# Kernel optimization log

Measured on AMD Instinct MI355X. Metric: run time of the kernel, lower is better.

The kernel has to match this reference:

```python
import jax, jax.numpy as jnp
import numpy as np

B, N, H = 8, 256, 64
L = 2          # n_layers
A = 10         # n_actions
EPS = 1e-5


def _layernorm(x, g, b):
    m = jnp.mean(x, axis=-1, keepdims=True)
    v = jnp.mean(jnp.square(x - m), axis=-1, keepdims=True)
    return (x - m) * jax.lax.rsqrt(v + EPS) * g + b


def setup_inputs() -> dict:
    key = jax.random.key(0)
    ks = jax.random.split(key, 12)
    s = 0.05
    return {
        "X": jax.random.normal(ks[0], (B, N, H), dtype=jnp.float32),
        "E": jax.random.normal(ks[1], (B, N, N, H), dtype=jnp.float32),
        # per-layer weights, stacked over layers (torch Linear: y = x @ W.T)
        "W3": jax.random.normal(ks[2], (L, H, H), dtype=jnp.float32) * s,
        "W4": jax.random.normal(ks[3], (L, H, H), dtype=jnp.float32) * s,
        "W5": jax.random.normal(ks[4], (L, H, H), dtype=jnp.float32) * s,
        "W6": jax.random.normal(ks[5], (L, H, H), dtype=jnp.float32) * s,
        "ln_ng": jnp.ones((L, H), dtype=jnp.float32),
        "ln_nb": jnp.zeros((L, H), dtype=jnp.float32),
        "ln_eg": jnp.ones((L, H), dtype=jnp.float32),
        "ln_eb": jnp.zeros((L, H), dtype=jnp.float32),
        "hw1": jax.random.normal(ks[6], (H, H), dtype=jnp.float32) * s,
        "hb1": jnp.zeros((H,), dtype=jnp.float32),
        "hw2": jax.random.normal(ks[7], (A, H), dtype=jnp.float32) * s,
        "hb2": jnp.zeros((A,), dtype=jnp.float32),
    }


def reference(X, E, W3, W4, W5, W6, ln_ng, ln_nb, ln_eg, ln_eb, hw1, hb1, hw2, hb2):
    # in_proj / edge_proj are Identity (in_dim == edge_dim == hid_dim)
    for l in range(L):
        Xi = X @ W3[l].T                       # (B,n,H)
        E_hat = E @ W4[l].T                    # (B,n,n,H)
        # (Xi_exp + Xj_exp + E_hat).sum(-1) == Xi.sum(-1)[:,:,None] + Xi.sum(-1)[:,None,:] + E_hat.sum(-1)
        s = jnp.sum(Xi, axis=-1)               # (B,n)
        att_logits = s[:, :, None] + s[:, None, :] + jnp.sum(E_hat, axis=-1)
        att = jax.nn.softmax(att_logits, axis=-1)[..., None]  # (B,n,n,1)
        E_next = E_hat * att                   # (B,n,n,H)
        Xj = X @ W5[l].T                       # (B,n,H)
        agg = jnp.einsum('bijh,bjh->bih', E_next, Xj)
        X_res = X @ W6[l].T
        X = _layernorm(jax.nn.relu(agg + X_res), ln_ng[l], ln_nb[l]) + X
        E = _layernorm(E_next, ln_eg[l], ln_eb[l])
        # dropout p=0.0 -> identity
    h = jax.nn.relu(X @ hw1.T + hb1)
    return h @ hw2.T + hb2                     # (B,n,n_actions)
```

## Files before the change

kernel.cpp:

```cpp
#include <hip/hip_runtime.h>
#include <hip/hip_bf16.h>

#define NB 256
#define HH 64

using short8 = __attribute__((ext_vector_type(8))) short;
using f4     = __attribute__((ext_vector_type(4))) float;

static __device__ __forceinline__ unsigned short f2bfbits(float f) {
    __hip_bfloat16 h = __float2bfloat16(f);
    return __builtin_bit_cast(unsigned short, h);
}

static __device__ __forceinline__ void split8(const float* v, short8& hi, short8& lo) {
    unsigned int hd[4], ld[4];
    #pragma unroll
    for (int j = 0; j < 4; ++j) {
        unsigned int u0 = __builtin_bit_cast(unsigned int, v[2*j]);
        unsigned int u1 = __builtin_bit_cast(unsigned int, v[2*j+1]);
        hd[j] = (u1 & 0xFFFF0000u) | (u0 >> 16);
        float r0 = v[2*j]   - __builtin_bit_cast(float, u0 & 0xFFFF0000u);
        float r1 = v[2*j+1] - __builtin_bit_cast(float, u1 & 0xFFFF0000u);
        ld[j] = ((unsigned int)f2bfbits(r1) << 16) | (unsigned int)f2bfbits(r0);
    }
    uint4 h4; h4.x = hd[0]; h4.y = hd[1]; h4.z = hd[2]; h4.w = hd[3];
    uint4 l4; l4.x = ld[0]; l4.y = ld[1]; l4.z = ld[2]; l4.w = ld[3];
    hi = __builtin_bit_cast(short8, h4);
    lo = __builtin_bit_cast(short8, l4);
}

static __device__ __forceinline__ short8 ld_frag_pair(const char* base, int idx0) {
    uint2 a = *reinterpret_cast<const uint2*>(base + (size_t)idx0 * 8);
    uint2 b = *reinterpret_cast<const uint2*>(base + (size_t)idx0 * 8 + 128);
    uint4 u; u.x = a.x; u.y = a.y; u.z = b.x; u.w = b.y;
    return __builtin_bit_cast(short8, u);
}

__global__ __launch_bounds__(256)
void setup_kernel(const float* __restrict__ W3, const float* __restrict__ W4,
                  float* __restrict__ w3s, uint4* __restrict__ w4tab) {
    const int t = threadIdx.x;
    if (blockIdx.x == 0) {
        if (t < 128) {
            const int l = t >> 6, k = t & 63;
            float s = 0.f;
            for (int h = 0; h < 64; ++h) s += W3[(size_t)(l*64 + h)*64 + k];
            w3s[t] = s;
        }
    } else {
        const int l = blockIdx.x - 1;
        const float* W4l = W4 + (size_t)l * 4096;
        uint4* tab = w4tab + (size_t)l * 1024;
        const int mt = t >> 6, lane = t & 63, m = lane & 15, q = lane >> 4;
        const float* row = W4l + (size_t)(mt*16 + m) * 64;
        #pragma unroll
        for (int ks = 0; ks < 2; ++ks) {
            float v[8];
            *reinterpret_cast<float4*>(&v[0]) = *reinterpret_cast<const float4*>(row + ks*32 + q*8);
            *reinterpret_cast<float4*>(&v[4]) = *reinterpret_cast<const float4*>(row + ks*32 + q*8 + 4);
            short8 hi, lo;
            split8(v, hi, lo);
            tab[(mt*4 + ks)*64 + lane]     = __builtin_bit_cast(uint4, hi);
            tab[(mt*4 + 2 + ks)*64 + lane] = __builtin_bit_cast(uint4, lo);
        }
    }
}

__global__ __launch_bounds__(256)
void prep_kernel(const float* __restrict__ Xsrc,
                 const float* __restrict__ w3s,
                 const float* __restrict__ W5l,
                 const float* __restrict__ W6l,
                 float* __restrict__ s_ws,
                 float* __restrict__ Xjf,
                 float* __restrict__ Xres_ws)
{
    __shared__ float w5s[64*65];
    __shared__ float w6s[64*65];
    const int t = threadIdx.x;
    #pragma unroll
    for (int j = 0; j < 4; ++j) {
        const int fidx = j*1024 + t*4;
        float4 v5 = *reinterpret_cast<const float4*>(W5l + fidx);
        float4 v6 = *reinterpret_cast<const float4*>(W6l + fidx);
        const int row = fidx >> 6, col = fidx & 63;
        w5s[row*65+col+0] = v5.x; w5s[row*65+col+1] = v5.y;
        w5s[row*65+col+2] = v5.z; w5s[row*65+col+3] = v5.w;
        w6s[row*65+col+0] = v6.x; w6s[row*65+col+1] = v6.y;
        w6s[row*65+col+2] = v6.z; w6s[row*65+col+3] = v6.w;
    }
    __syncthreads();

    const int w = t >> 6, lane = t & 63;
    const int r = blockIdx.x * 4 + w;
    float xr[64];
    #pragma unroll
    for (int k = 0; k < 16; ++k) {
        float4 v = *reinterpret_cast<const float4*>(Xsrc + (size_t)r*64 + k*4);
        xr[k*4+0] = v.x; xr[k*4+1] = v.y; xr[k*4+2] = v.z; xr[k*4+3] = v.w;
    }
    float aj = 0.f, ar = 0.f;
    #pragma unroll
    for (int k = 0; k < 64; ++k) {
        aj += xr[k] * w5s[lane*65 + k];
        ar += xr[k] * w6s[lane*65 + k];
    }
    const int b = r >> 8, j = r & 255;
    const int wj = j >> 6, jt = (j >> 4) & 3, m = j & 15;
    const int mt = lane >> 4, q = (lane >> 2) & 3, ri = lane & 3;
    Xjf[(size_t)b*16384 + (size_t)(((wj*4 + jt)*4 + mt)*64 + (q*16 + m))*4 + ri] = aj;
    Xres_ws[(size_t)r*64 + lane] = ar;
    float sv = xr[lane] * w3s[lane];
    #pragma unroll
    for (int d = 1; d < 64; d <<= 1) sv += __shfl_xor(sv, d, 64);
    if (lane == 0) s_ws[r] = sv;
}

template<bool FIRST>
__global__ __launch_bounds__(256)
void layer_kernel(void* Ebuf,
                  const float* __restrict__ s_ws,
                  const float* __restrict__ Xjf,
                  const float* __restrict__ Xres_ws,
                  const float* __restrict__ Xold,
                  float* __restrict__ Xnext,
                  const uint4* __restrict__ w4tab,
                  const float* __restrict__ eg,
                  const float* __restrict__ eb,
                  const float* __restrict__ ng,
                  const float* __restrict__ nb)
{
    __shared__ float att[NB];
    __shared__ float red[8];
    __shared__ float agg_lds[4][64];

    const int bi  = blockIdx.x;
    const int b   = bi >> 8;
    const int tid = threadIdx.x;
    const int w   = tid >> 6;
    const int lane = tid & 63;
    const int m = lane & 15;
    const int q = lane >> 4;

    char* ebase = (char*)Ebuf + (size_t)bi * 65536;

    short8 aH[4][2], aL[4][2];
    #pragma unroll
    for (int mt = 0; mt < 4; ++mt) {
        aH[mt][0] = __builtin_bit_cast(short8, w4tab[(mt*4 + 0)*64 + lane]);
        aH[mt][1] = __builtin_bit_cast(short8, w4tab[(mt*4 + 1)*64 + lane]);
        aL[mt][0] = __builtin_bit_cast(short8, w4tab[(mt*4 + 2)*64 + lane]);
        aL[mt][1] = __builtin_bit_cast(short8, w4tab[(mt*4 + 3)*64 + lane]);
    }

    f4 acc[4][4] = {};

    #pragma unroll
    for (int jt = 0; jt < 4; ++jt) {
        short8 bh0, bl0, bh1, bl1;
        if constexpr (FIRST) {
            const float* er = (const float*)ebase + (size_t)(w*64 + jt*16 + m) * 64;
            float v0[8], v1[8];
            *reinterpret_cast<float4*>(&v0[0]) = *reinterpret_cast<const float4*>(er + q*8);
            *reinterpret_cast<float4*>(&v0[4]) = *reinterpret_cast<const float4*>(er + q*8 + 4);
            *reinterpret_cast<float4*>(&v1[0]) = *reinterpret_cast<const float4*>(er + 32 + q*8);
            *reinterpret_cast<float4*>(&v1[4]) = *reinterpret_cast<const float4*>(er + 32 + q*8 + 4);
            split8(v0, bh0, bl0);
            split8(v1, bh1, bl1);
        } else {
            const char* hiP = ebase;
            const char* loP = ebase + 32768;
            const int col = (q & 1)*32 + m;
            const int base0 = ((w*4 + jt)*4)*64;
            const int mt0 = (q >> 1);
            bh0 = ld_frag_pair(hiP, base0 + mt0*64 + col);
            bh1 = ld_frag_pair(hiP, base0 + (2 + mt0)*64 + col);
            bl0 = ld_frag_pair(loP, base0 + mt0*64 + col);
            bl1 = ld_frag_pair(loP, base0 + (2 + mt0)*64 + col);
        }
        #pragma unroll
        for (int mt = 0; mt < 4; ++mt) {
            acc[mt][jt] = __builtin_amdgcn_mfma_f32_16x16x32_bf16(aH[mt][0], bh0, acc[mt][jt], 0, 0, 0);
            acc[mt][jt] = __builtin_amdgcn_mfma_f32_16x16x32_bf16(aL[mt][0], bh0, acc[mt][jt], 0, 0, 0);
            acc[mt][jt] = __builtin_amdgcn_mfma_f32_16x16x32_bf16(aH[mt][0], bl0, acc[mt][jt], 0, 0, 0);
            acc[mt][jt] = __builtin_amdgcn_mfma_f32_16x16x32_bf16(aH[mt][1], bh1, acc[mt][jt], 0, 0, 0);
            acc[mt][jt] = __builtin_amdgcn_mfma_f32_16x16x32_bf16(aL[mt][1], bh1, acc[mt][jt], 0, 0, 0);
            acc[mt][jt] = __builtin_amdgcn_mfma_f32_16x16x32_bf16(aH[mt][1], bl1, acc[mt][jt], 0, 0, 0);
        }
    }

    #pragma unroll
    for (int jt = 0; jt < 4; ++jt) {
        float t = 0.f;
        #pragma unroll
        for (int mt = 0; mt < 4; ++mt)
            #pragma unroll
            for (int r = 0; r < 4; ++r) t += acc[mt][jt][r];
        t += __shfl_xor(t, 16, 64);
        t += __shfl_xor(t, 32, 64);
        if (lane < 16) att[w*64 + jt*16 + lane] = t;
    }
    __syncthreads();

    const float lj = att[tid] + s_ws[bi] + s_ws[b*NB + tid];
    float mx = lj;
    #pragma unroll
    for (int d = 1; d < 64; d <<= 1) mx = fmaxf(mx, __shfl_xor(mx, d, 64));
    if (lane == 0) red[w] = mx;
    __syncthreads();
    mx = fmaxf(fmaxf(red[0], red[1]), fmaxf(red[2], red[3]));
    const float ev = __expf(lj - mx);
    float sm = ev;
    #pragma unroll
    for (int d = 1; d < 64; d <<= 1) sm += __shfl_xor(sm, d, 64);
    if (lane == 0) red[4 + w] = sm;
    __syncthreads();
    sm = (red[4] + red[5]) + (red[6] + red[7]);
    att[tid] = ev / sm;
    __syncthreads();

    float attv[4];
    #pragma unroll
    for (int jt = 0; jt < 4; ++jt) attv[jt] = att[w*64 + jt*16 + m];
    #pragma unroll
    for (int mt = 0; mt < 4; ++mt)
        #pragma unroll
        for (int jt = 0; jt < 4; ++jt)
            #pragma unroll
            for (int r = 0; r < 4; ++r) acc[mt][jt][r] *= attv[jt];

    float mean[4], rstd[4];
    #pragma unroll
    for (int jt = 0; jt < 4; ++jt) {
        float s = 0.f, ss = 0.f;
        #pragma unroll
        for (int mt = 0; mt < 4; ++mt)
            #pragma unroll
            for (int r = 0; r < 4; ++r) { float v = acc[mt][jt][r]; s += v; ss += v*v; }
        s  += __shfl_xor(s, 16, 64);  s  += __shfl_xor(s, 32, 64);
        ss += __shfl_xor(ss, 16, 64); ss += __shfl_xor(ss, 32, 64);
        float mu = s * (1.f/64.f);
        mean[jt] = mu;
        rstd[jt] = rsqrtf(ss * (1.f/64.f) - mu*mu + 1e-5f);
    }

    float p[4][4] = {};
    #pragma unroll
    for (int jt = 0; jt < 4; ++jt) {
        #pragma unroll
        for (int mt = 0; mt < 4; ++mt) {
            float4 xv = *reinterpret_cast<const float4*>(
                Xjf + (size_t)b*16384 + (size_t)(((w*4 + jt)*4 + mt)*64 + lane)*4);
            p[mt][0] += acc[mt][jt][0] * xv.x;
            p[mt][1] += acc[mt][jt][1] * xv.y;
            p[mt][2] += acc[mt][jt][2] * xv.z;
            p[mt][3] += acc[mt][jt][3] * xv.w;
        }
    }
    #pragma unroll
    for (int d = 1; d < 16; d <<= 1)
        #pragma unroll
        for (int mt = 0; mt < 4; ++mt)
            #pragma unroll
            for (int r = 0; r < 4; ++r) p[mt][r] += __shfl_xor(p[mt][r], d, 64);
    if (m == 0) {
        #pragma unroll
        for (int mt = 0; mt < 4; ++mt) {
            float4 st = make_float4(p[mt][0], p[mt][1], p[mt][2], p[mt][3]);
            *reinterpret_cast<float4*>(&agg_lds[w][mt*16 + q*4]) = st;
        }
    }

    if constexpr (FIRST) {
        float egv[4][4], ebv[4][4];
        #pragma unroll
        for (int mt = 0; mt < 4; ++mt)
            #pragma unroll
            for (int r = 0; r < 4; ++r) {
                const int h = mt*16 + q*4 + r;
                egv[mt][r] = eg[h];
                ebv[mt][r] = eb[h];
            }
        char* hiP = ebase;
        char* loP = ebase + 32768;
        #pragma unroll
        for (int jt = 0; jt < 4; ++jt) {
            #pragma unroll
            for (int mt = 0; mt < 4; ++mt) {
                float o[4];
                #pragma unroll
                for (int r = 0; r < 4; ++r)
                    o[r] = (acc[mt][jt][r] - mean[jt]) * rstd[jt] * egv[mt][r] + ebv[mt][r];
                unsigned int u0 = __builtin_bit_cast(unsigned int, o[0]);
                unsigned int u1 = __builtin_bit_cast(unsigned int, o[1]);
                unsigned int u2 = __builtin_bit_cast(unsigned int, o[2]);
                unsigned int u3 = __builtin_bit_cast(unsigned int, o[3]);
                uint2 h2;
                h2.x = (u1 & 0xFFFF0000u) | (u0 >> 16);
                h2.y = (u3 & 0xFFFF0000u) | (u2 >> 16);
                float r0 = o[0] - __builtin_bit_cast(float, u0 & 0xFFFF0000u);
                float r1 = o[1] - __builtin_bit_cast(float, u1 & 0xFFFF0000u);
                float r2 = o[2] - __builtin_bit_cast(float, u2 & 0xFFFF0000u);
                float r3 = o[3] - __builtin_bit_cast(float, u3 & 0xFFFF0000u);
                uint2 l2;
                l2.x = ((unsigned int)f2bfbits(r1) << 16) | (unsigned int)f2bfbits(r0);
                l2.y = ((unsigned int)f2bfbits(r3) << 16) | (unsigned int)f2bfbits(r2);
                const int idxS = ((w*4 + jt)*4 + mt)*64 + lane;
                *reinterpret_cast<uint2*>(hiP + (size_t)idxS*8) = h2;
                *reinterpret_cast<uint2*>(loP + (size_t)idxS*8) = l2;
            }
        }
    }
    __syncthreads();

    if (w == 0) {
        float a = agg_lds[0][lane] + agg_lds[1][lane] + agg_lds[2][lane] + agg_lds[3][lane];
        float v = fmaxf(a + Xres_ws[(size_t)bi*64 + lane], 0.f);
        float s = v, ss = v*v;
        #pragma unroll
        for (int d = 1; d < 64; d <<= 1) { s += __shfl_xor(s, d, 64); ss += __shfl_xor(ss, d, 64); }
        float mu  = s * (1.f/64.f);
        float var = ss * (1.f/64.f) - mu*mu;
        Xnext[(size_t)bi*64 + lane] =
            (v - mu) * rsqrtf(var + 1e-5f) * ng[lane] + nb[lane] + Xold[(size_t)bi*64 + lane];
    }
}

__global__ __launch_bounds__(256)
void head_kernel(const float* __restrict__ Xf,
                 const float* __restrict__ hw1,
                 const float* __restrict__ hb1,
                 const float* __restrict__ hw2,
                 const float* __restrict__ hb2,
                 float* __restrict__ out)
{
    __shared__ float w1s[64*65];
    __shared__ float w2s[10*65];
    __shared__ float h1s[4][64];
    const int t = threadIdx.x;
    #pragma unroll
    for (int j = 0; j < 4; ++j) {
        const int fidx = j*1024 + t*4;
        float4 v = *reinterpret_cast<const float4*>(hw1 + fidx);
        const int row = fidx >> 6, col = fidx & 63;
        w1s[row*65+col+0] = v.x; w1s[row*65+col+1] = v.y;
        w1s[row*65+col+2] = v.z; w1s[row*65+col+3] = v.w;
    }
    if (t < 160) {
        const int fidx = t*4;
        float4 v = *reinterpret_cast<const float4*>(hw2 + fidx);
        const int row = fidx >> 6, col = fidx & 63;
        w2s[row*65+col+0] = v.x; w2s[row*65+col+1] = v.y;
        w2s[row*65+col+2] = v.z; w2s[row*65+col+3] = v.w;
    }
    __syncthreads();

    const int w = t >> 6, lane = t & 63;
    const int r = blockIdx.x * 4 + w;
    float xr[64];
    #pragma unroll
    for (int k = 0; k < 16; ++k) {
        float4 v = *reinterpret_cast<const float4*>(Xf + (size_t)r*64 + k*4);
        xr[k*4+0] = v.x; xr[k*4+1] = v.y; xr[k*4+2] = v.z; xr[k*4+3] = v.w;
    }
    float a = hb1[lane];
    #pragma unroll
    for (int k = 0; k < 64; ++k) a += xr[k] * w1s[lane*65 + k];
    h1s[w][lane] = fmaxf(a, 0.f);
    __syncthreads();
    if (lane < 10) {
        float o = hb2[lane];
        #pragma unroll
        for (int h = 0; h < 64; ++h) o += h1s[w][h] * w2s[lane*65 + h];
        out[(size_t)r*10 + lane] = o;
    }
}

extern "C" void kernel_launch(void* const* d_in, const int* in_sizes, int n_in,
                              void* d_out, int out_size, void* d_ws, size_t ws_size,
                              hipStream_t stream) {
    const float* X   = (const float*)d_in[0];
    void*        E   = (void*)d_in[1];
    const float* W3  = (const float*)d_in[2];
    const float* W4  = (const float*)d_in[3];
    const float* W5  = (const float*)d_in[4];
    const float* W6  = (const float*)d_in[5];
    const float* ng  = (const float*)d_in[6];
    const float* nbp = (const float*)d_in[7];
    const float* eg  = (const float*)d_in[8];
    const float* ebp = (const float*)d_in[9];
    const float* hw1 = (const float*)d_in[10];
    const float* hb1 = (const float*)d_in[11];
    const float* hw2 = (const float*)d_in[12];
    const float* hb2 = (const float*)d_in[13];
    float* outp = (float*)d_out;

    float* wsf   = (float*)d_ws;
    float* s_ws  = wsf;
    float* Xjf   = wsf + 2048;
    float* Xres  = wsf + 133120;
    float* Xa    = wsf + 264192;
    float* Xb    = wsf + 395264;
    float* w3s   = wsf + 526336;
    uint4* w4tab = (uint4*)(wsf + 526464);

    setup_kernel<<<3, 256, 0, stream>>>(W3, W4, w3s, w4tab);

    prep_kernel<<<512, 256, 0, stream>>>(X, w3s, W5, W6, s_ws, Xjf, Xres);
    layer_kernel<true><<<2048, 256, 0, stream>>>(E, s_ws, Xjf, Xres,
        X, Xa, w4tab, eg, ebp, ng, nbp);

    prep_kernel<<<512, 256, 0, stream>>>(Xa, w3s + 64, W5 + 4096, W6 + 4096,
        s_ws, Xjf, Xres);
    layer_kernel<false><<<2048, 256, 0, stream>>>(E, s_ws, Xjf, Xres,
        Xa, Xb, w4tab + 1024, eg + 64, ebp + 64, ng + 64, nbp + 64);

    head_kernel<<<512, 256, 0, stream>>>(Xb, hw1, hb1, hw2, hb2, outp);
}
```

Baseline: 309.4 us.

## Store layer-1 edges as single bf16, precompute layer-2 logits, fuse head and setup

Layer 1 now writes its normalized edge tensor back as a single bf16 copy instead of hi/lo split pairs, laid out so layer 2 can load fragments with one 16-byte load each. Layer 1 also computes the layer-2 attention logit row-sum directly, using column sums of W4[1]. Layer 2 therefore skips the logit reduction, the lo-part MFMAs and the edge LayerNorm, since its E output is never used. The setup kernel is folded into the first prep launch and the head MLP into the last layer kernel. Together this cuts E traffic, MFMA count and launch count, at the cost of reduced precision for layer-2 edges, which are rounded once to bf16.

```diff
diff --git a/kernel.cpp b/kernel.cpp
--- a/kernel.cpp
+++ b/kernel.cpp
@@ -11,16 +11,20 @@
     __hip_bfloat16 h = __float2bfloat16(f);
     return __builtin_bit_cast(unsigned short, h);
 }
+static __device__ __forceinline__ float bfbits2f(unsigned short u) {
+    unsigned int x = (unsigned int)u << 16;
+    return __builtin_bit_cast(float, x);
+}
 
 static __device__ __forceinline__ void split8(const float* v, short8& hi, short8& lo) {
     unsigned int hd[4], ld[4];
     #pragma unroll
     for (int j = 0; j < 4; ++j) {
-        unsigned int u0 = __builtin_bit_cast(unsigned int, v[2*j]);
-        unsigned int u1 = __builtin_bit_cast(unsigned int, v[2*j+1]);
-        hd[j] = (u1 & 0xFFFF0000u) | (u0 >> 16);
-        float r0 = v[2*j]   - __builtin_bit_cast(float, u0 & 0xFFFF0000u);
-        float r1 = v[2*j+1] - __builtin_bit_cast(float, u1 & 0xFFFF0000u);
+        unsigned short h0 = f2bfbits(v[2*j]);
+        unsigned short h1 = f2bfbits(v[2*j+1]);
+        hd[j] = ((unsigned int)h1 << 16) | (unsigned int)h0;
+        float r0 = v[2*j]   - bfbits2f(h0);
+        float r1 = v[2*j+1] - bfbits2f(h1);
         ld[j] = ((unsigned int)f2bfbits(r1) << 16) | (unsigned int)f2bfbits(r0);
     }
     uint4 h4; h4.x = hd[0]; h4.y = hd[1]; h4.z = hd[2]; h4.w = hd[3];
@@ -29,29 +33,31 @@
     lo = __builtin_bit_cast(short8, l4);
 }
 
-static __device__ __forceinline__ short8 ld_frag_pair(const char* base, int idx0) {
-    uint2 a = *reinterpret_cast<const uint2*>(base + (size_t)idx0 * 8);
-    uint2 b = *reinterpret_cast<const uint2*>(base + (size_t)idx0 * 8 + 128);
-    uint4 u; u.x = a.x; u.y = a.y; u.z = b.x; u.w = b.y;
-    return __builtin_bit_cast(short8, u);
-}
-
+template<bool BUILD>
 __global__ __launch_bounds__(256)
-void setup_kernel(const float* __restrict__ W3, const float* __restrict__ W4,
-                  float* __restrict__ w3s, uint4* __restrict__ w4tab) {
+void prep_kernel(const float* __restrict__ Xsrc,
+                 const float* __restrict__ W3l,
+                 const float* __restrict__ W5l,
+                 const float* __restrict__ W6l,
+                 const float* __restrict__ W4all,
+                 uint4* __restrict__ w4tab,
+                 float* __restrict__ w41cs,
+                 float* __restrict__ s_ws,
+                 float* __restrict__ Xjf,
+                 float* __restrict__ Xres_ws)
+{
+    __shared__ float w5s[64*65];
+    __shared__ float w6s[64*65];
+    __shared__ float csl[4][64];
+    __shared__ float cst[64];
     const int t = threadIdx.x;
-    if (blockIdx.x == 0) {
-        if (t < 128) {
-            const int l = t >> 6, k = t & 63;
-            float s = 0.f;
-            for (int h = 0; h < 64; ++h) s += W3[(size_t)(l*64 + h)*64 + k];
-            w3s[t] = s;
-        }
-    } else {
-        const int l = blockIdx.x - 1;
-        const float* W4l = W4 + (size_t)l * 4096;
+    const int w = t >> 6, lane = t & 63;
+
+    if (BUILD && blockIdx.x >= 512) {
+        const int l = blockIdx.x - 512;
+        const float* W4l = W4all + (size_t)l * 4096;
         uint4* tab = w4tab + (size_t)l * 1024;
-        const int mt = t >> 6, lane = t & 63, m = lane & 15, q = lane >> 4;
+        const int mt = w, m = lane & 15, q = lane >> 4;
         const float* row = W4l + (size_t)(mt*16 + m) * 64;
         #pragma unroll
         for (int ks = 0; ks < 2; ++ks) {
@@ -63,24 +69,20 @@
             tab[(mt*4 + ks)*64 + lane]     = __builtin_bit_cast(uint4, hi);
             tab[(mt*4 + 2 + ks)*64 + lane] = __builtin_bit_cast(uint4, lo);
         }
-    }
-}
-
-__global__ __launch_bounds__(256)
-void prep_kernel(const float* __restrict__ Xsrc,
-                 const float* __restrict__ w3s,
-                 const float* __restrict__ W5l,
-                 const float* __restrict__ W6l,
-                 float* __restrict__ s_ws,
-                 float* __restrict__ Xjf,
-                 float* __restrict__ Xres_ws)
-{
-    __shared__ float w5s[64*65];
-    __shared__ float w6s[64*65];
-    const int t = threadIdx.x;
-    #pragma unroll
-    for (int j = 0; j < 4; ++j) {
-        const int fidx = j*1024 + t*4;
+        if (l == 1) {
+            float p = 0.f;
+            #pragma unroll
+            for (int i = 0; i < 16; ++i) p += W4l[(size_t)(w*16 + i)*64 + lane];
+            csl[w][lane] = p;
+            __syncthreads();
+            if (t < 64) w41cs[t] = (csl[0][t] + csl[1][t]) + (csl[2][t] + csl[3][t]);
+        }
+        return;
+    }
+
+    #pragma unroll
+    for (int jj = 0; jj < 4; ++jj) {
+        const int fidx = jj*1024 + t*4;
         float4 v5 = *reinterpret_cast<const float4*>(W5l + fidx);
         float4 v6 = *reinterpret_cast<const float4*>(W6l + fidx);
         const int row = fidx >> 6, col = fidx & 63;
@@ -89,9 +91,14 @@
         w6s[row*65+col+0] = v6.x; w6s[row*65+col+1] = v6.y;
         w6s[row*65+col+2] = v6.z; w6s[row*65+col+3] = v6.w;
     }
-    __syncthreads();
-
-    const int w = t >> 6, lane = t & 63;
+    float pcs = 0.f;
+    #pragma unroll
+    for (int i = 0; i < 16; ++i) pcs += W3l[(size_t)(w*16 + i)*64 + lane];
+    csl[w][lane] = pcs;
+    __syncthreads();
+    if (t < 64) cst[t] = (csl[0][t] + csl[1][t]) + (csl[2][t] + csl[3][t]);
+    __syncthreads();
+
     const int r = blockIdx.x * 4 + w;
     float xr[64];
     #pragma unroll
@@ -110,13 +117,13 @@
     const int mt = lane >> 4, q = (lane >> 2) & 3, ri = lane & 3;
     Xjf[(size_t)b*16384 + (size_t)(((wj*4 + jt)*4 + mt)*64 + (q*16 + m))*4 + ri] = aj;
     Xres_ws[(size_t)r*64 + lane] = ar;
-    float sv = xr[lane] * w3s[lane];
+    float sv = xr[lane] * cst[lane];
     #pragma unroll
     for (int d = 1; d < 64; d <<= 1) sv += __shfl_xor(sv, d, 64);
     if (lane == 0) s_ws[r] = sv;
 }
 
-template<bool FIRST>
+template<bool FIRST, bool LAST>
 __global__ __launch_bounds__(256)
 void layer_kernel(void* Ebuf,
                   const float* __restrict__ s_ws,
@@ -125,14 +132,22 @@
                   const float* __restrict__ Xold,
                   float* __restrict__ Xnext,
                   const uint4* __restrict__ w4tab,
+                  const float* __restrict__ w41cs,
                   const float* __restrict__ eg,
                   const float* __restrict__ eb,
                   const float* __restrict__ ng,
-                  const float* __restrict__ nb)
+                  const float* __restrict__ nb,
+                  const float* __restrict__ hw1,
+                  const float* __restrict__ hb1,
+                  const float* __restrict__ hw2,
+                  const float* __restrict__ hb2,
+                  float* __restrict__ outp)
 {
     __shared__ float att[NB];
     __shared__ float red[8];
     __shared__ float agg_lds[4][64];
+    __shared__ float w1s[LAST ? 64*65 : 1];
+    __shared__ float w2s[LAST ? 10*65 : 1];
 
     const int bi  = blockIdx.x;
     const int b   = bi >> 8;
@@ -144,65 +159,109 @@
 
     char* ebase = (char*)Ebuf + (size_t)bi * 65536;
 
-    short8 aH[4][2], aL[4][2];
+    float4 rawf[FIRST ? 4 : 1][FIRST ? 4 : 1];
+    uint4  rawb[FIRST ? 1 : 4][FIRST ? 1 : 2];
+    if constexpr (FIRST) {
+        #pragma unroll
+        for (int jt = 0; jt < 4; ++jt) {
+            const float* er = (const float*)ebase + (size_t)(w*64 + jt*16 + m) * 64;
+            rawf[jt][0] = *reinterpret_cast<const float4*>(er + q*8);
+            rawf[jt][1] = *reinterpret_cast<const float4*>(er + q*8 + 4);
+            rawf[jt][2] = *reinterpret_cast<const float4*>(er + 32 + q*8);
+            rawf[jt][3] = *reinterpret_cast<const float4*>(er + 32 + q*8 + 4);
+        }
+    } else {
+        #pragma unroll
+        for (int jt = 0; jt < 4; ++jt)
+            #pragma unroll
+            for (int ks = 0; ks < 2; ++ks)
+                rawb[jt][ks] = *reinterpret_cast<const uint4*>(
+                    ebase + (size_t)(((w*4 + jt)*2 + ks)*64 + lane) * 16);
+    }
+
+    if constexpr (LAST) {
+        #pragma unroll
+        for (int jj = 0; jj < 4; ++jj) {
+            const int fidx = jj*1024 + tid*4;
+            float4 v = *reinterpret_cast<const float4*>(hw1 + fidx);
+            const int row = fidx >> 6, col = fidx & 63;
+            w1s[row*65+col+0] = v.x; w1s[row*65+col+1] = v.y;
+            w1s[row*65+col+2] = v.z; w1s[row*65+col+3] = v.w;
+        }
+        if (tid < 160) {
+            const int fidx = tid*4;
+            float4 v = *reinterpret_cast<const float4*>(hw2 + fidx);
+            const int row = fidx >> 6, col = fidx & 63;
+            w2s[row*65+col+0] = v.x; w2s[row*65+col+1] = v.y;
+            w2s[row*65+col+2] = v.z; w2s[row*65+col+3] = v.w;
+        }
+    }
+
+    short8 aH[4][2];
+    short8 aL[FIRST ? 4 : 1][FIRST ? 2 : 1];
     #pragma unroll
     for (int mt = 0; mt < 4; ++mt) {
         aH[mt][0] = __builtin_bit_cast(short8, w4tab[(mt*4 + 0)*64 + lane]);
         aH[mt][1] = __builtin_bit_cast(short8, w4tab[(mt*4 + 1)*64 + lane]);
-        aL[mt][0] = __builtin_bit_cast(short8, w4tab[(mt*4 + 2)*64 + lane]);
-        aL[mt][1] = __builtin_bit_cast(short8, w4tab[(mt*4 + 3)*64 + lane]);
+        if constexpr (FIRST) {
+            aL[mt][0] = __builtin_bit_cast(short8, w4tab[(mt*4 + 2)*64 + lane]);
+            aL[mt][1] = __builtin_bit_cast(short8, w4tab[(mt*4 + 3)*64 + lane]);
+        }
     }
 
     f4 acc[4][4] = {};
 
     #pragma unroll
     for (int jt = 0; jt < 4; ++jt) {
-        short8 bh0, bl0, bh1, bl1;
         if constexpr (FIRST) {
-            const float* er = (const float*)ebase + (size_t)(w*64 + jt*16 + m) * 64;
+            short8 bh0, bl0, bh1, bl1;
             float v0[8], v1[8];
-            *reinterpret_cast<float4*>(&v0[0]) = *reinterpret_cast<const float4*>(er + q*8);
-            *reinterpret_cast<float4*>(&v0[4]) = *reinterpret_cast<const float4*>(er + q*8 + 4);
-            *reinterpret_cast<float4*>(&v1[0]) = *reinterpret_cast<const float4*>(er + 32 + q*8);
-            *reinterpret_cast<float4*>(&v1[4]) = *reinterpret_cast<const float4*>(er + 32 + q*8 + 4);
+            *reinterpret_cast<float4*>(&v0[0]) = rawf[jt][0];
+            *reinterpret_cast<float4*>(&v0[4]) = rawf[jt][1];
+            *reinterpret_cast<float4*>(&v1[0]) = rawf[jt][2];
+            *reinterpret_cast<float4*>(&v1[4]) = rawf[jt][3];
             split8(v0, bh0, bl0);
             split8(v1, bh1, bl1);
+            #pragma unroll
+            for (int mt = 0; mt < 4; ++mt) {
+                acc[mt][jt] = __builtin_amdgcn_mfma_f32_16x16x32_bf16(aH[mt][0], bh0, acc[mt][jt], 0, 0, 0);
+                acc[mt][jt] = __builtin_amdgcn_mfma_f32_16x16x32_bf16(aL[mt][0], bh0, acc[mt][jt], 0, 0, 0);
+                acc[mt][jt] = __builtin_amdgcn_mfma_f32_16x16x32_bf16(aH[mt][0], bl0, acc[mt][jt], 0, 0, 0);
+                acc[mt][jt] = __builtin_amdgcn_mfma_f32_16x16x32_bf16(aH[mt][1], bh1, acc[mt][jt], 0, 0, 0);
+                acc[mt][jt] = __builtin_amdgcn_mfma_f32_16x16x32_bf16(aL[mt][1], bh1, acc[mt][jt], 0, 0, 0);
+                acc[mt][jt] = __builtin_amdgcn_mfma_f32_16x16x32_bf16(aH[mt][1], bl1, acc[mt][jt], 0, 0, 0);
+            }
         } else {
-            const char* hiP = ebase;
-            const char* loP = ebase + 32768;
-            const int col = (q & 1)*32 + m;
-            const int base0 = ((w*4 + jt)*4)*64;
-            const int mt0 = (q >> 1);
-            bh0 = ld_frag_pair(hiP, base0 + mt0*64 + col);
-            bh1 = ld_frag_pair(hiP, base0 + (2 + mt0)*64 + col);
-            bl0 = ld_frag_pair(loP, base0 + mt0*64 + col);
-            bl1 = ld_frag_pair(loP, base0 + (2 + mt0)*64 + col);
-        }
-        #pragma unroll
-        for (int mt = 0; mt < 4; ++mt) {
-            acc[mt][jt] = __builtin_amdgcn_mfma_f32_16x16x32_bf16(aH[mt][0], bh0, acc[mt][jt], 0, 0, 0);
-            acc[mt][jt] = __builtin_amdgcn_mfma_f32_16x16x32_bf16(aL[mt][0], bh0, acc[mt][jt], 0, 0, 0);
-            acc[mt][jt] = __builtin_amdgcn_mfma_f32_16x16x32_bf16(aH[mt][0], bl0, acc[mt][jt], 0, 0, 0);
-            acc[mt][jt] = __builtin_amdgcn_mfma_f32_16x16x32_bf16(aH[mt][1], bh1, acc[mt][jt], 0, 0, 0);
-            acc[mt][jt] = __builtin_amdgcn_mfma_f32_16x16x32_bf16(aL[mt][1], bh1, acc[mt][jt], 0, 0, 0);
-            acc[mt][jt] = __builtin_amdgcn_mfma_f32_16x16x32_bf16(aH[mt][1], bl1, acc[mt][jt], 0, 0, 0);
-        }
-    }
-
-    #pragma unroll
-    for (int jt = 0; jt < 4; ++jt) {
-        float t = 0.f;
-        #pragma unroll
-        for (int mt = 0; mt < 4; ++mt)
-            #pragma unroll
-            for (int r = 0; r < 4; ++r) t += acc[mt][jt][r];
-        t += __shfl_xor(t, 16, 64);
-        t += __shfl_xor(t, 32, 64);
-        if (lane < 16) att[w*64 + jt*16 + lane] = t;
-    }
-    __syncthreads();
-
-    const float lj = att[tid] + s_ws[bi] + s_ws[b*NB + tid];
+            short8 b0 = __builtin_bit_cast(short8, rawb[jt][0]);
+            short8 b1 = __builtin_bit_cast(short8, rawb[jt][1]);
+            #pragma unroll
+            for (int mt = 0; mt < 4; ++mt) {
+                acc[mt][jt] = __builtin_amdgcn_mfma_f32_16x16x32_bf16(aH[mt][0], b0, acc[mt][jt], 0, 0, 0);
+                acc[mt][jt] = __builtin_amdgcn_mfma_f32_16x16x32_bf16(aH[mt][1], b1, acc[mt][jt], 0, 0, 0);
+            }
+        }
+    }
+
+    float lj;
+    if constexpr (FIRST) {
+        #pragma unroll
+        for (int jt = 0; jt < 4; ++jt) {
+            float t = 0.f;
+            #pragma unroll
+            for (int mt = 0; mt < 4; ++mt)
+                #pragma unroll
+                for (int r = 0; r < 4; ++r) t += acc[mt][jt][r];
+            t += __shfl_xor(t, 16, 64);
+            t += __shfl_xor(t, 32, 64);
+            if (lane < 16) att[w*64 + jt*16 + lane] = t;
+        }
+        __syncthreads();
+        lj = att[tid] + s_ws[bi] + s_ws[b*NB + tid];
+    } else {
+        const float* t1g = (const float*)(ebase + 32768);
+        lj = t1g[tid] + s_ws[bi] + s_ws[b*NB + tid];
+    }
+
     float mx = lj;
     #pragma unroll
     for (int d = 1; d < 64; d <<= 1) mx = fmaxf(mx, __shfl_xor(mx, d, 64));
@@ -228,21 +287,6 @@
         for (int jt = 0; jt < 4; ++jt)
             #pragma unroll
             for (int r = 0; r < 4; ++r) acc[mt][jt][r] *= attv[jt];
-
-    float mean[4], rstd[4];
-    #pragma unroll
-    for (int jt = 0; jt < 4; ++jt) {
-        float s = 0.f, ss = 0.f;
-        #pragma unroll
-        for (int mt = 0; mt < 4; ++mt)
-            #pragma unroll
-            for (int r = 0; r < 4; ++r) { float v = acc[mt][jt][r]; s += v; ss += v*v; }
-        s  += __shfl_xor(s, 16, 64);  s  += __shfl_xor(s, 32, 64);
-        ss += __shfl_xor(ss, 16, 64); ss += __shfl_xor(ss, 32, 64);
-        float mu = s * (1.f/64.f);
-        mean[jt] = mu;
-        rstd[jt] = rsqrtf(ss * (1.f/64.f) - mu*mu + 1e-5f);
-    }
 
     float p[4][4] = {};
     #pragma unroll
@@ -272,43 +316,56 @@
     }
 
     if constexpr (FIRST) {
-        float egv[4][4], ebv[4][4];
+        float mean[4], rstd[4];
+        #pragma unroll
+        for (int jt = 0; jt < 4; ++jt) {
+            float s = 0.f, ss = 0.f;
+            #pragma unroll
+            for (int mt = 0; mt < 4; ++mt)
+                #pragma unroll
+                for (int r = 0; r < 4; ++r) { float v = acc[mt][jt][r]; s += v; ss += v*v; }
+            s  += __shfl_xor(s, 16, 64);  s  += __shfl_xor(s, 32, 64);
+            ss += __shfl_xor(ss, 16, 64); ss += __shfl_xor(ss, 32, 64);
+            float mu = s * (1.f/64.f);
+            mean[jt] = mu;
+            rstd[jt] = rsqrtf(ss * (1.f/64.f) - mu*mu + 1e-5f);
+        }
+        float egv[4][4], ebv[4][4], wcs[4][4];
         #pragma unroll
         for (int mt = 0; mt < 4; ++mt)
             #pragma unroll
             for (int r = 0; r < 4; ++r) {
-                const int h = mt*16 + q*4 + r;
-                egv[mt][r] = eg[h];
-                ebv[mt][r] = eb[h];
+                const int c = mt*16 + q*4 + r;
+                egv[mt][r] = eg[c];
+                ebv[mt][r] = eb[c];
+                wcs[mt][r] = w41cs[c];
             }
-        char* hiP = ebase;
-        char* loP = ebase + 32768;
+        float* t1g = (float*)(ebase + 32768);
+        float t1p[4] = {0.f, 0.f, 0.f, 0.f};
         #pragma unroll
         for (int jt = 0; jt < 4; ++jt) {
             #pragma unroll
             for (int mt = 0; mt < 4; ++mt) {
                 float o[4];
                 #pragma unroll
-                for (int r = 0; r < 4; ++r)
+                for (int r = 0; r < 4; ++r) {
                     o[r] = (acc[mt][jt][r] - mean[jt]) * rstd[jt] * egv[mt][r] + ebv[mt][r];
-                unsigned int u0 = __builtin_bit_cast(unsigned int, o[0]);
-                unsigned int u1 = __builtin_bit_cast(unsigned int, o[1]);
-                unsigned int u2 = __builtin_bit_cast(unsigned int, o[2]);
-                unsigned int u3 = __builtin_bit_cast(unsigned int, o[3]);
-                uint2 h2;
-                h2.x = (u1 & 0xFFFF0000u) | (u0 >> 16);
-                h2.y = (u3 & 0xFFFF0000u) | (u2 >> 16);
-                float r0 = o[0] - __builtin_bit_cast(float, u0 & 0xFFFF0000u);
-                float r1 = o[1] - __builtin_bit_cast(float, u1 & 0xFFFF0000u);
-                float r2 = o[2] - __builtin_bit_cast(float, u2 & 0xFFFF0000u);
-                float r3 = o[3] - __builtin_bit_cast(float, u3 & 0xFFFF0000u);
-                uint2 l2;
-                l2.x = ((unsigned int)f2bfbits(r1) << 16) | (unsigned int)f2bfbits(r0);
-                l2.y = ((unsigned int)f2bfbits(r3) << 16) | (unsigned int)f2bfbits(r2);
-                const int idxS = ((w*4 + jt)*4 + mt)*64 + lane;
-                *reinterpret_cast<uint2*>(hiP + (size_t)idxS*8) = h2;
-                *reinterpret_cast<uint2*>(loP + (size_t)idxS*8) = l2;
+                    t1p[jt] += o[r] * wcs[mt][r];
+                }
+                uint2 u2;
+                u2.x = ((unsigned int)f2bfbits(o[1]) << 16) | (unsigned int)f2bfbits(o[0]);
+                u2.y = ((unsigned int)f2bfbits(o[3]) << 16) | (unsigned int)f2bfbits(o[2]);
+                const int qp = (2*mt + (q >> 1)) & 3;
+                const size_t addr = (size_t)(((w*4 + jt)*2 + (mt >> 1))*64 + qp*16 + m)*16 + (q & 1)*8;
+                *reinterpret_cast<uint2*>(ebase + addr) = u2;
             }
+        }
+        #pragma unroll
+        for (int jt = 0; jt < 4; ++jt) {
+            float tv = t1p[jt];
+            tv += __shfl_xor(tv, 16, 64);
+            tv += __shfl_xor(tv, 32, 64);
+            if (lane < 16) t1g[w*64 + jt*16 + lane] = tv;
         }
     }
     __syncthreads();
@@ -321,58 +378,23 @@
         for (int d = 1; d < 64; d <<= 1) { s += __shfl_xor(s, d, 64); ss += __shfl_xor(ss, d, 64); }
         float mu  = s * (1.f/64.f);
         float var = ss * (1.f/64.f) - mu*mu;
-        Xnext[(size_t)bi*64 + lane] =
-            (v - mu) * rsqrtf(var + 1e-5f) * ng[lane] + nb[lane] + Xold[(size_t)bi*64 + lane];
-    }
-}
-
-__global__ __launch_bounds__(256)
-void head_kernel(const float* __restrict__ Xf,
-                 const float* __restrict__ hw1,
-                 const float* __restrict__ hb1,
-                 const float* __restrict__ hw2,
-                 const float* __restrict__ hb2,
-                 float* __restrict__ out)
-{
-    __shared__ float w1s[64*65];
-    __shared__ float w2s[10*65];
-    __shared__ float h1s[4][64];
-    const int t = threadIdx.x;
-    #pragma unroll
-    for (int j = 0; j < 4; ++j) {
-        const int fidx = j*1024 + t*4;
-        float4 v = *reinterpret_cast<const float4*>(hw1 + fidx);
-        const int row = fidx >> 6, col = fidx & 63;
-        w1s[row*65+col+0] = v.x; w1s[row*65+col+1] = v.y;
-        w1s[row*65+col+2] = v.z; w1s[row*65+col+3] = v.w;
-    }
-    if (t < 160) {
-        const int fidx = t*4;
-        float4 v = *reinterpret_cast<const float4*>(hw2 + fidx);
-        const int row = fidx >> 6, col = fidx & 63;
-        w2s[row*65+col+0] = v.x; w2s[row*65+col+1] = v.y;
-        w2s[row*65+col+2] = v.z; w2s[row*65+col+3] = v.w;
-    }
-    __syncthreads();
-
-    const int w = t >> 6, lane = t & 63;
-    const int r = blockIdx.x * 4 + w;
-    float xr[64];
-    #pragma unroll
-    for (int k = 0; k < 16; ++k) {
-        float4 v = *reinterpret_cast<const float4*>(Xf + (size_t)r*64 + k*4);
-        xr[k*4+0] = v.x; xr[k*4+1] = v.y; xr[k*4+2] = v.z; xr[k*4+3] = v.w;
-    }
-    float a = hb1[lane];
-    #pragma unroll
-    for (int k = 0; k < 64; ++k) a += xr[k] * w1s[lane*65 + k];
-    h1s[w][lane] = fmaxf(a, 0.f);
-    __syncthreads();
-    if (lane < 10) {
-        float o = hb2[lane];
-        #pragma unroll
-        for (int h = 0; h < 64; ++h) o += h1s[w][h] * w2s[lane*65 + h];
-        out[(size_t)r*10 + lane] = o;
+        float xfin = (v - mu) * rsqrtf(var + 1e-5f) * ng[lane] + nb[lane] + Xold[(size_t)bi*64 + lane];
+        if constexpr (!LAST) {
+            Xnext[(size_t)bi*64 + lane] = xfin;
+        } else {
+            att[lane] = xfin;
+            float h1 = hb1[lane];
+            #pragma unroll
+            for (int k = 0; k < 64; ++k) h1 += att[k] * w1s[lane*65 + k];
+            h1 = fmaxf(h1, 0.f);
+            att[64 + lane] = h1;
+            if (lane < 10) {
+                float o = hb2[lane];
+                #pragma unroll
+                for (int k = 0; k < 64; ++k) o += att[64 + k] * w2s[lane*65 + k];
+                outp[(size_t)bi*10 + lane] = o;
+            }
+        }
     }
 }
 
@@ -400,20 +422,18 @@
     float* Xjf   = wsf + 2048;
     float* Xres  = wsf + 133120;
     float* Xa    = wsf + 264192;
-    float* Xb    = wsf + 395264;
-    float* w3s   = wsf + 526336;
-    uint4* w4tab = (uint4*)(wsf + 526464);
-
-    setup_kernel<<<3, 256, 0, stream>>>(W3, W4, w3s, w4tab);
-
-    prep_kernel<<<512, 256, 0, stream>>>(X, w3s, W5, W6, s_ws, Xjf, Xres);
-    layer_kernel<true><<<2048, 256, 0, stream>>>(E, s_ws, Xjf, Xres,
-        X, Xa, w4tab, eg, ebp, ng, nbp);
-
-    prep_kernel<<<512, 256, 0, stream>>>(Xa, w3s + 64, W5 + 4096, W6 + 4096,
+    float* w41cs = wsf + 395264;
+    uint4* w4tab = (uint4*)(wsf + 395392);
+
+    prep_kernel<true><<<514, 256, 0, stream>>>(X, W3, W5, W6, W4, w4tab, w41cs,
         s_ws, Xjf, Xres);
-    layer_kernel<false><<<2048, 256, 0, stream>>>(E, s_ws, Xjf, Xres,
-        Xa, Xb, w4tab + 1024, eg + 64, ebp + 64, ng + 64, nbp + 64);
-
-    head_kernel<<<512, 256, 0, stream>>>(Xb, hw1, hb1, hw2, hb2, outp);
-}
+    layer_kernel<true, false><<<2048, 256, 0, stream>>>(E, s_ws, Xjf, Xres,
+        X, Xa, w4tab, w41cs, eg, ebp, ng, nbp,
+        nullptr, nullptr, nullptr, nullptr, nullptr);
+
+    prep_kernel<false><<<512, 256, 0, stream>>>(Xa, W3 + 4096, W5 + 4096, W6 + 4096,
+        nullptr, nullptr, nullptr, s_ws, Xjf, Xres);
+    layer_kernel<false, true><<<2048, 256, 0, stream>>>(E, s_ws, Xjf, Xres,
+        Xa, nullptr, w4tab + 1024, nullptr, nullptr, nullptr, ng + 64, nbp + 64,
+        hw1, hb1, hw2, hb2, outp);
+}
```

After: 291.1 us. 5.9% less time.
